# Kernel tuning notes

Hardware: AMD Instinct MI355X
Metric: run time of the kernel (lower is better)

Reference implementation:

```python
import jax, jax.numpy as jnp
import numpy as np

D_MODEL = 1024
N_HEADS = 16
D_HEAD = D_MODEL // N_HEADS
HIDDEN = 4096
B, T = 2, 2048
EPS = 1e-5


def setup_inputs() -> dict:
    key = jax.random.key(0)
    ks = jax.random.split(key, 16)
    s = 0.02
    return {
        "x": jax.random.normal(ks[0], (B, T, D_MODEL), dtype=jnp.float32),
        # LayerNorm 1
        "gamma1": jnp.ones((D_MODEL,), jnp.float32),
        "beta1": jnp.zeros((D_MODEL,), jnp.float32),
        # attention projections, stored (in, out) so y = x @ W + b
        "Wq": jax.random.normal(ks[1], (D_MODEL, D_MODEL), jnp.float32) * s,
        "bq": jnp.zeros((D_MODEL,), jnp.float32),
        "Wk": jax.random.normal(ks[2], (D_MODEL, D_MODEL), jnp.float32) * s,
        "bk": jnp.zeros((D_MODEL,), jnp.float32),
        "Wv": jax.random.normal(ks[3], (D_MODEL, D_MODEL), jnp.float32) * s,
        "bv": jnp.zeros((D_MODEL,), jnp.float32),
        "Wo": jax.random.normal(ks[4], (D_MODEL, D_MODEL), jnp.float32) * s,
        "bo": jnp.zeros((D_MODEL,), jnp.float32),
        # LayerNorm 2
        "gamma2": jnp.ones((D_MODEL,), jnp.float32),
        "beta2": jnp.zeros((D_MODEL,), jnp.float32),
        # MLP
        "W1": jax.random.normal(ks[5], (D_MODEL, HIDDEN), jnp.float32) * s,
        "b1": jnp.zeros((HIDDEN,), jnp.float32),
        "W2": jax.random.normal(ks[6], (HIDDEN, D_MODEL), jnp.float32) * s,
        "b2": jnp.zeros((D_MODEL,), jnp.float32),
    }


def _layernorm(x, gamma, beta):
    mean = jnp.mean(x, axis=-1, keepdims=True)
    var = jnp.mean(jnp.square(x - mean), axis=-1, keepdims=True)  # unbiased=False
    return gamma * (x - mean) * jax.lax.rsqrt(var + EPS) + beta


def _attention(x, Wq, bq, Wk, bk, Wv, bv, Wo, bo):
    b, t, _ = x.shape
    q = (x @ Wq + bq).reshape(b, t, N_HEADS, D_HEAD)
    k = (x @ Wk + bk).reshape(b, t, N_HEADS, D_HEAD)
    v = (x @ Wv + bv).reshape(b, t, N_HEADS, D_HEAD)
    scores = jnp.einsum("bqhd,bkhd->bhqk", q, k) / np.sqrt(D_HEAD).astype(np.float32)
    causal = jnp.tril(jnp.ones((t, t), dtype=bool))  # keep j <= i
    scores = jnp.where(causal, scores, -jnp.inf)
    attn = jax.nn.softmax(scores, axis=-1)
    out = jnp.einsum("bhqk,bkhd->bqhd", attn, v).reshape(b, t, D_MODEL)
    return out @ Wo + bo


def reference(x, gamma1, beta1, Wq, bq, Wk, bk, Wv, bv, Wo, bo,
              gamma2, beta2, W1, b1, W2, b2):
    # x = x + Attn(LN1(x))
    x = x + _attention(_layernorm(x, gamma1, beta1), Wq, bq, Wk, bk, Wv, bv, Wo, bo)
    # x = x + MLP(LN2(x)); torch F.gelu default = exact erf gelu
    h = _layernorm(x, gamma2, beta2)
    h = jax.nn.gelu(h @ W1 + b1, approximate=False) @ W2 + b2
    return x + h
```

## Files before the change

kernel.cpp:

```cpp
#include <hip/hip_runtime.h>
#include <stdint.h>

typedef unsigned short u16;
typedef short bf16x8 __attribute__((ext_vector_type(8)));
typedef float f32x4 __attribute__((ext_vector_type(4)));
typedef float f32x16 __attribute__((ext_vector_type(16)));

#define MB (1024L*1024L)

__device__ inline u16 f2bf(float f) {
  union { float f; unsigned u; } v; v.f = f;
  unsigned r = (v.u + 0x7FFFu + ((v.u >> 16) & 1u)) >> 16;
  return (u16)r;
}

__device__ inline float bf2f(u16 u) {
  union { unsigned u; float f; } v; v.u = ((unsigned)u) << 16; return v.f;
}

__device__ inline unsigned cvtpk(float lo, float hi) {
  unsigned r;
  asm("v_cvt_pk_bf16_f32 %0, %1, %2" : "=v"(r) : "v"(lo), "v"(hi));
  return r;
}

#define GLOAD16(gptr, lptr) \
  __builtin_amdgcn_global_load_lds((__attribute__((address_space(1))) void*)(gptr), \
                                   (__attribute__((address_space(3))) void*)(lptr), 16, 0, 0)

__global__ __launch_bounds__(256) void wprep(
    const float* __restrict__ Wq, const float* __restrict__ Wk,
    const float* __restrict__ Wv, const float* __restrict__ Wo,
    const float* __restrict__ W1, const float* __restrict__ W2,
    const float* __restrict__ bq, const float* __restrict__ bk,
    const float* __restrict__ bv,
    u16* __restrict__ WqkvT, u16* __restrict__ WoT,
    u16* __restrict__ W1T, u16* __restrict__ W2T, float* __restrict__ bqkv,
    const float* __restrict__ x, const float* __restrict__ gamma1,
    const float* __restrict__ beta1, u16* __restrict__ xn) {
  const int blk = blockIdx.x;
  const int tid = threadIdx.x;
  __shared__ float tile[32][33];
  __shared__ float red[8];

  if (blk >= 12292) {
    const int row = blk - 12292;
    const float4 v = *(const float4*)(x + (size_t)row * 1024 + tid * 4);
    float s = v.x + v.y + v.z + v.w;
    float s2 = v.x * v.x + v.y * v.y + v.z * v.z + v.w * v.w;
#pragma unroll
    for (int mm = 1; mm < 64; mm <<= 1) {
      s += __shfl_xor(s, mm, 64);
      s2 += __shfl_xor(s2, mm, 64);
    }
    const int w = tid >> 6;
    if ((tid & 63) == 0) { red[w] = s; red[4 + w] = s2; }
    __syncthreads();
    s = red[0] + red[1] + red[2] + red[3];
    s2 = red[4] + red[5] + red[6] + red[7];
    const float mean = s * (1.0f / 1024.0f);
    const float var = s2 * (1.0f / 1024.0f) - mean * mean;
    const float rstd = rsqrtf(var + 1e-5f);
    const float4 g = *(const float4*)(gamma1 + tid * 4);
    const float4 bb = *(const float4*)(beta1 + tid * 4);
    ushort4 o;
    o.x = f2bf(g.x * (v.x - mean) * rstd + bb.x);
    o.y = f2bf(g.y * (v.y - mean) * rstd + bb.y);
    o.z = f2bf(g.z * (v.z - mean) * rstd + bb.z);
    o.w = f2bf(g.w * (v.w - mean) * rstd + bb.w);
    *(ushort4*)(xn + (size_t)row * 1024 + tid * 4) = o;
    return;
  }
  if (blk >= 12288) {
    int i = (blk - 12288) * 256 + tid;
    bqkv[i] = bq[i]; bqkv[1024 + i] = bk[i]; bqkv[2048 + i] = bv[i];
    return;
  }
  const float* W; u16* WT; int K, N, tb;
  if (blk < 4096) {
    K = 1024; N = 1024;
    if (blk < 1024)      { W = Wq; WT = WqkvT;               tb = blk; }
    else if (blk < 2048) { W = Wk; WT = WqkvT + 1024 * 1024; tb = blk - 1024; }
    else if (blk < 3072) { W = Wv; WT = WqkvT + 2048 * 1024; tb = blk - 2048; }
    else                 { W = Wo; WT = WoT;                 tb = blk - 3072; }
  } else if (blk < 8192) { W = W1; WT = W1T; K = 1024; N = 4096; tb = blk - 4096; }
  else                   { W = W2; WT = W2T; K = 4096; N = 1024; tb = blk - 8192; }

  const int nbn = N >> 5;
  const int bk_ = tb / nbn;
  const int bn = tb % nbn;
  const int r = tid >> 3;
  const int c4 = (tid & 7) << 2;
  const float4 v = *(const float4*)(W + (size_t)(bk_ * 32 + r) * N + bn * 32 + c4);
  tile[r][c4 + 0] = v.x; tile[r][c4 + 1] = v.y;
  tile[r][c4 + 2] = v.z; tile[r][c4 + 3] = v.w;
  __syncthreads();
  ushort4 o;
  o.x = f2bf(tile[c4 + 0][r]); o.y = f2bf(tile[c4 + 1][r]);
  o.z = f2bf(tile[c4 + 2][r]); o.w = f2bf(tile[c4 + 3][r]);
  *(ushort4*)(WT + (size_t)(bn * 32 + r) * K + bk_ * 32 + c4) = o;
}

__global__ __launch_bounds__(256) void ln_kernel(const float* __restrict__ x,
                                                 const float* __restrict__ gamma,
                                                 const float* __restrict__ beta,
                                                 u16* __restrict__ out) {
  const int row = blockIdx.x;
  const int tid = threadIdx.x;
  const float4 v = *(const float4*)(x + (size_t)row * 1024 + tid * 4);
  float s = v.x + v.y + v.z + v.w;
  float s2 = v.x * v.x + v.y * v.y + v.z * v.z + v.w * v.w;
#pragma unroll
  for (int m = 1; m < 64; m <<= 1) {
    s += __shfl_xor(s, m, 64);
    s2 += __shfl_xor(s2, m, 64);
  }
  __shared__ float red[8];
  const int w = tid >> 6;
  if ((tid & 63) == 0) { red[w] = s; red[4 + w] = s2; }
  __syncthreads();
  s = red[0] + red[1] + red[2] + red[3];
  s2 = red[4] + red[5] + red[6] + red[7];
  const float mean = s * (1.0f / 1024.0f);
  const float var = s2 * (1.0f / 1024.0f) - mean * mean;
  const float rstd = rsqrtf(var + 1e-5f);
  const float4 g = *(const float4*)(gamma + tid * 4);
  const float4 b = *(const float4*)(beta + tid * 4);
  ushort4 o;
  o.x = f2bf(g.x * (v.x - mean) * rstd + b.x);
  o.y = f2bf(g.y * (v.y - mean) * rstd + b.y);
  o.z = f2bf(g.z * (v.z - mean) * rstd + b.z);
  o.w = f2bf(g.w * (v.w - mean) * rstd + b.w);
  *(ushort4*)(out + (size_t)row * 1024 + tid * 4) = o;
}

template <int EPI>
__global__ __launch_bounds__(512, 1)
void gemm256sq(const u16* __restrict__ A, const u16* __restrict__ BT,
               const float* __restrict__ bias, void* __restrict__ outp,
               int M, int N, int K) {
  __shared__ __align__(16) u16 As[2][256 * 64];
  __shared__ __align__(16) u16 Bs[2][256 * 64];
  const int nBN = N >> 8;
  const int blk = blockIdx.x;
  const int xcd = blk & 7;
  const int rr = blk >> 3;
  const int bm = xcd * 2 + rr / nBN;
  const int bn = rr % nBN;
  const int tid = threadIdx.x;
  const int lane = tid & 63;
  const int wid = tid >> 6;
  const int wm = wid >> 2;
  const int wn = wid & 3;
  const int e4 = lane >> 4;
  const int l15 = lane & 15;
  const int sx = l15 & 7;

  const int aoffb = (wm * 128 + l15) * 64;
  const int boffb = (wn * 64 + l15) * 64;
  const int ch0 = ((e4 ^ sx) & 7) << 3;
  const int ch1 = (((4 | e4) ^ sx) & 7) << 3;

  size_t gA[2], gB[2]; int lo[2];
#pragma unroll
  for (int c = 0; c < 2; ++c) {
    int idx = tid + (c << 9);
    int rowl = idx >> 3;
    int chg = ((idx & 7) ^ (rowl & 7)) << 3;
    gA[c] = (size_t)(bm * 256 + rowl) * K + chg;
    gB[c] = (size_t)(bn * 256 + rowl) * K + chg;
    lo[c] = idx << 4;
  }
  const size_t hK = (size_t)128 * K;

#define STG_A(tt, h) do { _Pragma("unroll") for (int c = 0; c < 2; ++c) \
  GLOAD16(A + gA[c] + (size_t)(h) * hK + (size_t)(tt) * 64, (char*)As[(tt) & 1] + (h) * 16384 + lo[c]); } while (0)
#define STG_B(tt, h) do { _Pragma("unroll") for (int c = 0; c < 2; ++c) \
  GLOAD16(BT + gB[c] + (size_t)(h) * hK + (size_t)(tt) * 64, (char*)Bs[(tt) & 1] + (h) * 16384 + lo[c]); } while (0)

  f32x4 acc[8][4] = {};
  const int nt = K >> 6;

  STG_A(0, 0); STG_A(0, 1); STG_B(0, 0); STG_B(0, 1);
  STG_B(1, 0); STG_B(1, 1);
  asm volatile("s_waitcnt vmcnt(4)" ::: "memory");
  __builtin_amdgcn_s_barrier();

  for (int t = 0; t < nt; ++t) {
    const u16* Ap = As[t & 1];
    const u16* Bp = Bs[t & 1];
    bf16x8 a[2][4], b01[2][2], b23[2][2];

#pragma unroll
    for (int mm = 0; mm < 4; ++mm) {
      a[0][mm] = *(const bf16x8*)(Ap + aoffb + mm * 1024 + ch0);
      a[1][mm] = *(const bf16x8*)(Ap + aoffb + mm * 1024 + ch1);
    }
#pragma unroll
    for (int nn = 0; nn < 2; ++nn) {
      b01[0][nn] = *(const bf16x8*)(Bp + boffb + nn * 1024 + ch0);
      b01[1][nn] = *(const bf16x8*)(Bp + boffb + nn * 1024 + ch1);
    }
    if (t + 1 < nt) STG_A(t + 1, 0);
    __builtin_amdgcn_s_barrier();
    asm volatile("s_waitcnt lgkmcnt(0)" ::: "memory");
    __builtin_amdgcn_s_setprio(1);
#pragma unroll
    for (int kk = 0; kk < 2; ++kk)
#pragma unroll
      for (int mm = 0; mm < 4; ++mm)
#pragma unroll
        for (int nn = 0; nn < 2; ++nn)
          acc[mm][nn] = __builtin_amdgcn_mfma_f32_16x16x32_bf16(a[kk][mm], b01[kk][nn], acc[mm][nn], 0, 0, 0);
    __builtin_amdgcn_s_setprio(0);
    __builtin_amdgcn_s_barrier();

#pragma unroll
    for (int nn = 0; nn < 2; ++nn) {
      b23[0][nn] = *(const bf16x8*)(Bp + boffb + (2 + nn) * 1024 + ch0);
      b23[1][nn] = *(const bf16x8*)(Bp + boffb + (2 + nn) * 1024 + ch1);
    }
    if (t + 1 < nt) STG_A(t + 1, 1);
    __builtin_amdgcn_s_barrier();
    asm volatile("s_waitcnt lgkmcnt(0)" ::: "memory");
    __builtin_amdgcn_s_setprio(1);
#pragma unroll
    for (int kk = 0; kk < 2; ++kk)
#pragma unroll
      for (int mm = 0; mm < 4; ++mm)
#pragma unroll
        for (int nn = 0; nn < 2; ++nn)
          acc[mm][2 + nn] = __builtin_amdgcn_mfma_f32_16x16x32_bf16(a[kk][mm], b23[kk][nn], acc[mm][2 + nn], 0, 0, 0);
    __builtin_amdgcn_s_setprio(0);
    __builtin_amdgcn_s_barrier();

#pragma unroll
    for (int mm = 0; mm < 4; ++mm) {
      a[0][mm] = *(const bf16x8*)(Ap + aoffb + (4 + mm) * 1024 + ch0);
      a[1][mm] = *(const bf16x8*)(Ap + aoffb + (4 + mm) * 1024 + ch1);
    }
    if (t + 2 < nt) STG_B(t + 2, 0);
    __builtin_amdgcn_s_barrier();
    asm volatile("s_waitcnt lgkmcnt(0)" ::: "memory");
    __builtin_amdgcn_s_setprio(1);
#pragma unroll
    for (int kk = 0; kk < 2; ++kk)
#pragma unroll
      for (int mm = 0; mm < 4; ++mm)
#pragma unroll
        for (int nn = 0; nn < 2; ++nn)
          acc[4 + mm][2 + nn] = __builtin_amdgcn_mfma_f32_16x16x32_bf16(a[kk][mm], b23[kk][nn], acc[4 + mm][2 + nn], 0, 0, 0);
    __builtin_amdgcn_s_setprio(0);
    __builtin_amdgcn_s_barrier();

    if (t + 2 < nt) STG_B(t + 2, 1);
    __builtin_amdgcn_s_barrier();
    __builtin_amdgcn_s_setprio(1);
#pragma unroll
    for (int kk = 0; kk < 2; ++kk)
#pragma unroll
      for (int mm = 0; mm < 4; ++mm)
#pragma unroll
        for (int nn = 0; nn < 2; ++nn)
          acc[4 + mm][nn] = __builtin_amdgcn_mfma_f32_16x16x32_bf16(a[kk][mm], b01[kk][nn], acc[4 + mm][nn], 0, 0, 0);
    __builtin_amdgcn_s_setprio(0);
    if (t + 1 < nt) {
      if (t + 2 < nt) asm volatile("s_waitcnt vmcnt(4)" ::: "memory");
      else            asm volatile("s_waitcnt vmcnt(0)" ::: "memory");
    }
    __builtin_amdgcn_s_barrier();
  }
#undef STG_A
#undef STG_B

  const int rbase = bm * 256 + wm * 128;
  const int cbase = bn * 256 + wn * 64;
#pragma unroll
  for (int m = 0; m < 8; ++m) {
#pragma unroll
    for (int n = 0; n < 4; ++n) {
      const int col = cbase + n * 16 + l15;
      const int row0 = rbase + m * 16 + e4 * 4;
      const float bv = bias[col];
#pragma unroll
      for (int r = 0; r < 4; ++r) {
        const int row = row0 + r;
        float v = acc[m][n][r] + bv;
        if (EPI == 2) {
          float tt = v * (1.0f + 0.044715f * v * v);
          float sg = 1.0f / (1.0f + __expf(-1.5957691216057308f * tt));
          ((u16*)outp)[(size_t)row * N + col] = f2bf(v * sg);
        } else {
          ((u16*)outp)[(size_t)row * N + col] = f2bf(v);
        }
      }
    }
  }
}

template <int EPI, int BN>
__global__ __launch_bounds__(256, (BN == 64) ? 3 : 2)
void gemm_bt(const u16* __restrict__ A, const u16* __restrict__ BT,
             const float* __restrict__ bias, const float* __restrict__ res,
             void* __restrict__ outp, int M, int N, int K) {
  constexpr int MF = (BN == 128) ? 4 : 2;
  constexpr int ACH = 4;
  constexpr int BCH = BN / 32;
  constexpr int LOADS = ACH + BCH;
  __shared__ __align__(16) u16 As[2][128 * 64];
  __shared__ __align__(16) u16 Bs[2][BN * 64];
  const int nBN = N / BN;
  const int hw = blockIdx.x;
  const int xcd = hw & 7;
  const int rr = hw >> 3;
  const int bm = xcd * 4 + rr / nBN;
  const int bn = rr % nBN;
  const int tid = threadIdx.x;
  const int lane = tid & 63;
  const int wid = tid >> 6;
  const int wm = (BN == 128) ? (wid >> 1) : wid;
  const int wn = (BN == 128) ? (wid & 1) : 0;
  const int e4 = lane >> 4;

  int abase[MF], ax[MF];
#pragma unroll
  for (int m = 0; m < MF; ++m) {
    int rowa = wm * (MF * 16) + m * 16 + (lane & 15);
    abase[m] = rowa * 64; ax[m] = rowa & 7;
  }
  int bbase[4], bx[4];
#pragma unroll
  for (int n = 0; n < 4; ++n) {
    int rowb = wn * 64 + n * 16 + (lane & 15);
    bbase[n] = rowb * 64; bx[n] = rowb & 7;
  }

  size_t ga[ACH]; int loa[ACH];
#pragma unroll
  for (int c = 0; c < ACH; ++c) {
    int idx = tid + (c << 8);
    int row = idx >> 3;
    int ch = (idx & 7) ^ (row & 7);
    ga[c] = (size_t)(bm * 128 + row) * K + (ch << 3);
    loa[c] = idx << 4;
  }
  size_t gb[BCH]; int lob[BCH];
#pragma unroll
  for (int c = 0; c < BCH; ++c) {
    int idx = tid + (c << 8);
    int row = idx >> 3;
    int ch = (idx & 7) ^ (row & 7);
    gb[c] = (size_t)(bn * BN + row) * K + (ch << 3);
    lob[c] = idx << 4;
  }

#define STAGE_G(t, bb) do { \
  _Pragma("unroll") for (int c = 0; c < ACH; ++c) \
    GLOAD16(A + ga[c] + (size_t)(t) * 64, (char*)As[bb] + loa[c]); \
  _Pragma("unroll") for (int c = 0; c < BCH; ++c) \
    GLOAD16(BT + gb[c] + (size_t)(t) * 64, (char*)Bs[bb] + lob[c]); \
} while (0)

  f32x4 acc[MF][4] = {};
  const int nt = K >> 6;

  STAGE_G(0, 0);
  STAGE_G(1, 1);

  for (int t = 0; t < nt; ++t) {
    if (t + 1 < nt) {
      asm volatile("s_waitcnt vmcnt(%0)" :: "i"(LOADS) : "memory");
    } else {
      asm volatile("s_waitcnt vmcnt(0)" ::: "memory");
    }
    __builtin_amdgcn_s_barrier();
    const u16* Ap = As[t & 1];
    const u16* Bp = Bs[t & 1];
    bf16x8 af[2][MF], bfr[2][4];
#pragma unroll
    for (int kk = 0; kk < 2; ++kk) {
#pragma unroll
      for (int m = 0; m < MF; ++m)
        af[kk][m] = *(const bf16x8*)(Ap + abase[m] + (((((kk << 2) | e4)) ^ ax[m]) << 3));
#pragma unroll
      for (int n = 0; n < 4; ++n)
        bfr[kk][n] = *(const bf16x8*)(Bp + bbase[n] + (((((kk << 2) | e4)) ^ bx[n]) << 3));
    }
    asm volatile("s_waitcnt lgkmcnt(0)" ::: "memory");
    __builtin_amdgcn_s_barrier();
    if (t + 2 < nt) STAGE_G(t + 2, t & 1);
    __builtin_amdgcn_s_setprio(1);
#pragma unroll
    for (int kk = 0; kk < 2; ++kk)
#pragma unroll
      for (int m = 0; m < MF; ++m)
#pragma unroll
        for (int n = 0; n < 4; ++n)
          acc[m][n] = __builtin_amdgcn_mfma_f32_16x16x32_bf16(af[kk][m], bfr[kk][n], acc[m][n], 0, 0, 0);
    __builtin_amdgcn_s_setprio(0);
  }
#undef STAGE_G

  const int rbase = bm * 128 + wm * (MF * 16);
  const int cbase = bn * BN + wn * 64;
#pragma unroll
  for (int m = 0; m < MF; ++m) {
#pragma unroll
    for (int n = 0; n < 4; ++n) {
      const int col = cbase + n * 16 + (lane & 15);
      const int row0 = rbase + m * 16 + ((lane >> 4) << 2);
      const float bv = bias[col];
#pragma unroll
      for (int r = 0; r < 4; ++r) {
        const int row = row0 + r;
        float v = acc[m][n][r] + bv;
        if (EPI == 1) {
          ((float*)outp)[(size_t)row * N + col] = v + res[(size_t)row * N + col];
        } else if (EPI == 2) {
          float tt = v * (1.0f + 0.044715f * v * v);
          float sg = 1.0f / (1.0f + __expf(-1.5957691216057308f * tt));
          ((u16*)outp)[(size_t)row * N + col] = f2bf(v * sg);
        } else {
          ((u16*)outp)[(size_t)row * N + col] = f2bf(v);
        }
      }
    }
  }
}

__global__ __launch_bounds__(256, 2) void attn_kernel(const u16* __restrict__ QKV,
                                                      u16* __restrict__ O) {
  __shared__ __align__(16) u16 KV[4][4096];
  const int T = 2048, LD = 3072;
  const int blk = blockIdx.x;
  const int xcd = blk & 7;
  const int bh = xcd * 4 + ((blk >> 3) & 3);
  const int c = 15 - (blk >> 5);
  const int b = bh >> 4, hd = bh & 15;
  const int tid = threadIdx.x;
  const int lane = tid & 63;
  const int w = tid >> 6;
  const int h = lane >> 5;
  const int qg = c * 128 + w * 32 + (lane & 31);
  const int diag = 2 * c + (w >> 1);
  const int myNt = diag + 1;
  const int nt = 2 * c + 2;

  const u16* Qb = QKV + (size_t)b * T * LD + hd * 64;
  const u16* Kb = Qb + 1024;
  const u16* Vb = Qb + 2048;

  const float QSC = 0.18033688011112042f;
  bf16x8 qf[4];
#pragma unroll
  for (int s = 0; s < 4; ++s) {
    bf16x8 raw = *(const bf16x8*)(Qb + (size_t)qg * LD + s * 16 + h * 8);
    union { unsigned wd[4]; bf16x8 v; } u;
#pragma unroll
    for (int e = 0; e < 4; ++e)
      u.wd[e] = cvtpk(bf2f((u16)raw[2 * e]) * QSC, bf2f((u16)raw[2 * e + 1]) * QSC);
    qf[s] = u.v;
  }

  union PF { unsigned wd[4]; bf16x8 v; } ONES;
  ONES.wd[0] = 0x3F803F80u; ONES.wd[1] = 0x3F803F80u;
  ONES.wd[2] = 0x3F803F80u; ONES.wd[3] = 0x3F803F80u;

  f32x16 oacc[2] = {};
  f32x16 lacc = {};

  int krow[2], kgc[2], vrow[2], vcol[2];
#pragma unroll
  for (int c2 = 0; c2 < 2; ++c2) {
    int i2 = tid + (c2 << 8);
    krow[c2] = i2 >> 3;
    kgc[c2] = ((i2 & 7) ^ (krow[c2] & 7)) << 3;
    vrow[c2] = i2 >> 3;
    vcol[c2] = i2 & 7;
  }

#define VWRITE(buf, c2, vvreg) do { \
  _Pragma("unroll") for (int e = 0; e < 8; ++e) { \
    int d = vcol[c2] * 8 + e; \
    KV[2 + (buf)][(d << 6) | (vrow[c2] & 7) | ((((vrow[c2] >> 3) ^ e ^ vcol[c2]) & 7) << 3)] = (u16)(vvreg)[e]; \
  } \
} while (0)

#pragma unroll
  for (int c2 = 0; c2 < 2; ++c2) {
    GLOAD16(Kb + (size_t)krow[c2] * LD + kgc[c2], (char*)KV[0] + (tid + (c2 << 8)) * 16);
    bf16x8 vv0 = *(const bf16x8*)(Vb + (size_t)vrow[c2] * LD + vcol[c2] * 8);
    VWRITE(0, c2, vv0);
  }
  __syncthreads();

  int cur = 0;
  for (int j = 0; j < nt; ++j) {
    const bool pre = (j + 1 < nt);
    bf16x8 vv[2];
    if (pre) {
#pragma unroll
      for (int c2 = 0; c2 < 2; ++c2) {
        GLOAD16(Kb + (size_t)((j + 1) * 64 + krow[c2]) * LD + kgc[c2],
                (char*)KV[cur ^ 1] + (tid + (c2 << 8)) * 16);
        vv[c2] = *(const bf16x8*)(Vb + (size_t)((j + 1) * 64 + vrow[c2]) * LD + vcol[c2] * 8);
      }
    }

    if (j < myNt) {
      f32x16 sacc[2];
#pragma unroll
      for (int t = 0; t < 2; ++t)
#pragma unroll
        for (int r = 0; r < 16; ++r) sacc[t][r] = -8.0f;
      const u16* Kp = KV[cur];
      __builtin_amdgcn_s_setprio(1);
#pragma unroll
      for (int t = 0; t < 2; ++t) {
#pragma unroll
        for (int s = 0; s < 4; ++s) {
          int row = t * 32 + (lane & 31);
          bf16x8 kf = *(const bf16x8*)(Kp + (row << 6) + ((((2 * s + h) ^ (row & 7)) & 7) << 3));
          sacc[t] = __builtin_amdgcn_mfma_f32_32x32x16_bf16(kf, qf[s], sacc[t], 0, 0, 0);
        }
      }
      __builtin_amdgcn_s_setprio(0);

      if (j == diag) {
#pragma unroll
        for (int t = 0; t < 2; ++t)
#pragma unroll
          for (int r = 0; r < 16; ++r) {
            int key = (j << 6) + 32 * t + (r & 3) + 8 * (r >> 2) + 4 * h;
            if (key > qg) sacc[t][r] = -200.0f;
          }
      }

#pragma unroll
      for (int t = 0; t < 2; ++t)
#pragma unroll
        for (int r = 0; r < 16; ++r)
          sacc[t][r] = exp2f(sacc[t][r]);

      union PF pf[4];
#pragma unroll
      for (int t = 0; t < 2; ++t) {
#pragma unroll
        for (int kb = 0; kb < 2; ++kb) {
          int base = 8 * kb;
          unsigned A0 = cvtpk(sacc[t][base + 0], sacc[t][base + 1]);
          unsigned A2 = cvtpk(sacc[t][base + 2], sacc[t][base + 3]);
          unsigned A4 = cvtpk(sacc[t][base + 4], sacc[t][base + 5]);
          unsigned A6 = cvtpk(sacc[t][base + 6], sacc[t][base + 7]);
          unsigned S0 = (unsigned)__shfl_xor((int)(h ? A0 : A4), 32, 64);
          unsigned S2 = (unsigned)__shfl_xor((int)(h ? A2 : A6), 32, 64);
          PF& u = pf[2 * t + kb];
          u.wd[0] = h ? S0 : A0;
          u.wd[1] = h ? S2 : A2;
          u.wd[2] = h ? A4 : S0;
          u.wd[3] = h ? A6 : S2;
        }
      }

      const u16* Vp = KV[2 + cur];
      __builtin_amdgcn_s_setprio(1);
#pragma unroll
      for (int ks = 0; ks < 4; ++ks) {
#pragma unroll
        for (int d2 = 0; d2 < 2; ++d2) {
          int d = d2 * 32 + (lane & 31);
          bf16x8 vf = *(const bf16x8*)(Vp + (d << 6) + ((((2 * ks + h) ^ (d & 7) ^ ((d >> 3) & 7)) & 7) << 3));
          oacc[d2] = __builtin_amdgcn_mfma_f32_32x32x16_bf16(vf, pf[ks].v, oacc[d2], 0, 0, 0);
        }
        lacc = __builtin_amdgcn_mfma_f32_32x32x16_bf16(ONES.v, pf[ks].v, lacc, 0, 0, 0);
      }
      __builtin_amdgcn_s_setprio(0);
    }

    if (pre) {
#pragma unroll
      for (int c2 = 0; c2 < 2; ++c2) VWRITE(cur ^ 1, c2, vv[c2]);
    }
    __syncthreads();
    cur ^= 1;
  }
#undef VWRITE

  const float rinv = 1.0f / lacc[0];
  u16* Ob = (u16*)KV;
  const int qloc = w * 32 + (lane & 31);
#pragma unroll
  for (int d2 = 0; d2 < 2; ++d2)
#pragma unroll
    for (int r = 0; r < 16; ++r) {
      int d = d2 * 32 + (r & 3) + 8 * (r >> 2) + 4 * h;
      Ob[(qloc << 6) | (d ^ ((qloc & 7) << 3))] = f2bf(oacc[d2][r] * rinv);
    }
  __syncthreads();
#pragma unroll
  for (int it = 0; it < 4; ++it) {
    int r = (tid >> 3) + it * 32;
    int c8 = tid & 7;
    bf16x8 val = *(const bf16x8*)(Ob + (r << 6) + (((c8 ^ (r & 7)) & 7) << 3));
    int qg2 = c * 128 + r;
    *(bf16x8*)(O + (size_t)(b * T + qg2) * 1024 + hd * 64 + c8 * 8) = val;
  }
}

extern "C" void kernel_launch(void* const* d_in, const int* in_sizes, int n_in,
                              void* d_out, int out_size, void* d_ws, size_t ws_size,
                              hipStream_t stream) {
  const float* x      = (const float*)d_in[0];
  const float* gamma1 = (const float*)d_in[1];
  const float* beta1  = (const float*)d_in[2];
  const float* Wq     = (const float*)d_in[3];
  const float* bq     = (const float*)d_in[4];
  const float* Wk     = (const float*)d_in[5];
  const float* bk     = (const float*)d_in[6];
  const float* Wv     = (const float*)d_in[7];
  const float* bv     = (const float*)d_in[8];
  const float* Wo     = (const float*)d_in[9];
  const float* bo     = (const float*)d_in[10];
  const float* gamma2 = (const float*)d_in[11];
  const float* beta2  = (const float*)d_in[12];
  const float* W1     = (const float*)d_in[13];
  const float* b1     = (const float*)d_in[14];
  const float* W2     = (const float*)d_in[15];
  const float* b2     = (const float*)d_in[16];

  char* ws = (char*)d_ws;
  u16* WqkvT = (u16*)(ws + 0 * MB);
  u16* WoT   = (u16*)(ws + 6 * MB);
  u16* W1T   = (u16*)(ws + 8 * MB);
  u16* W2T   = (u16*)(ws + 16 * MB);
  u16* qkv   = (u16*)(ws + 24 * MB);
  u16* hb    = (u16*)(ws + 24 * MB);
  u16* xn    = (u16*)(ws + 56 * MB);
  float* bqkv = (float*)d_out;
  float* x1 = (float*)d_out;

  const int M = 4096;

  wprep<<<dim3(16388), dim3(256), 0, stream>>>(Wq, Wk, Wv, Wo, W1, W2, bq, bk, bv,
                                               WqkvT, WoT, W1T, W2T, bqkv,
                                               x, gamma1, beta1, xn);

  gemm256sq<0><<<dim3(192), dim3(512), 0, stream>>>(xn, WqkvT, bqkv, qkv, M, 3072, 1024);

  attn_kernel<<<dim3(512), dim3(256), 0, stream>>>(qkv, xn);

  gemm_bt<1, 64><<<dim3(512), dim3(256), 0, stream>>>(xn, WoT, bo, x, x1, M, 1024, 1024);

  ln_kernel<<<dim3(M), dim3(256), 0, stream>>>(x1, gamma2, beta2, xn);

  gemm256sq<2><<<dim3(256), dim3(512), 0, stream>>>(xn, W1T, b1, hb, M, 4096, 1024);
  gemm_bt<1, 64><<<dim3(512), dim3(256), 0, stream>>>(hb, W2T, b2, x1, d_out, M, 1024, 4096);
}
```

Before: 217.5 us.

## Split causal attention KV loop across two blocks and merge partials

Each query chunk's key tiles are split between two blocks by even and odd tile index. This doubles the attention grid for better occupancy and load balance. Because softmax uses a fixed max offset, the unnormalized partial outputs and row sums can be added in a new merge kernel that normalizes and writes the final layout. The score init also seeds the first MFMA with a constant accumulator. The cost is an extra launch, bf16 partial round-trips through memory (reusing d_out as scratch), and some precision loss from storing unnormalized partials in bf16.

```diff
diff --git a/kernel.cpp b/kernel.cpp
--- a/kernel.cpp
+++ b/kernel.cpp
@@ -428,14 +428,18 @@
   }
 }
 
-__global__ __launch_bounds__(256, 2) void attn_kernel(const u16* __restrict__ QKV,
-                                                      u16* __restrict__ O) {
+__global__ __launch_bounds__(256, 2) void attn_split(const u16* __restrict__ QKV,
+                                                     u16* __restrict__ Opart,
+                                                     float* __restrict__ Lpart) {
   __shared__ __align__(16) u16 KV[4][4096];
   const int T = 2048, LD = 3072;
   const int blk = blockIdx.x;
   const int xcd = blk & 7;
-  const int bh = xcd * 4 + ((blk >> 3) & 3);
-  const int c = 15 - (blk >> 5);
+  const int q9 = blk >> 3;
+  const int bh = xcd * 4 + (q9 & 3);
+  const int rest = q9 >> 2;
+  const int s = rest & 1;
+  const int c = 15 - (rest >> 1);
   const int b = bh >> 4, hd = bh & 15;
   const int tid = threadIdx.x;
   const int lane = tid & 63;
@@ -444,7 +448,7 @@
   const int qg = c * 128 + w * 32 + (lane & 31);
   const int diag = 2 * c + (w >> 1);
   const int myNt = diag + 1;
-  const int nt = 2 * c + 2;
+  const int ntc = 2 * c + 2;
 
   const u16* Qb = QKV + (size_t)b * T * LD + hd * 64;
   const u16* Kb = Qb + 1024;
@@ -453,18 +457,22 @@
   const float QSC = 0.18033688011112042f;
   bf16x8 qf[4];
 #pragma unroll
-  for (int s = 0; s < 4; ++s) {
-    bf16x8 raw = *(const bf16x8*)(Qb + (size_t)qg * LD + s * 16 + h * 8);
+  for (int ss = 0; ss < 4; ++ss) {
+    bf16x8 raw = *(const bf16x8*)(Qb + (size_t)qg * LD + ss * 16 + h * 8);
     union { unsigned wd[4]; bf16x8 v; } u;
 #pragma unroll
     for (int e = 0; e < 4; ++e)
       u.wd[e] = cvtpk(bf2f((u16)raw[2 * e]) * QSC, bf2f((u16)raw[2 * e + 1]) * QSC);
-    qf[s] = u.v;
+    qf[ss] = u.v;
   }
 
   union PF { unsigned wd[4]; bf16x8 v; } ONES;
   ONES.wd[0] = 0x3F803F80u; ONES.wd[1] = 0x3F803F80u;
   ONES.wd[2] = 0x3F803F80u; ONES.wd[3] = 0x3F803F80u;
+
+  f32x16 NEG8;
+#pragma unroll
+  for (int r = 0; r < 16; ++r) NEG8[r] = -8.0f;
 
   f32x16 oacc[2] = {};
   f32x16 lacc = {};
@@ -488,40 +496,40 @@
 
 #pragma unroll
   for (int c2 = 0; c2 < 2; ++c2) {
-    GLOAD16(Kb + (size_t)krow[c2] * LD + kgc[c2], (char*)KV[0] + (tid + (c2 << 8)) * 16);
-    bf16x8 vv0 = *(const bf16x8*)(Vb + (size_t)vrow[c2] * LD + vcol[c2] * 8);
+    GLOAD16(Kb + (size_t)(s * 64 + krow[c2]) * LD + kgc[c2], (char*)KV[0] + (tid + (c2 << 8)) * 16);
+    bf16x8 vv0 = *(const bf16x8*)(Vb + (size_t)(s * 64 + vrow[c2]) * LD + vcol[c2] * 8);
     VWRITE(0, c2, vv0);
   }
   __syncthreads();
 
   int cur = 0;
-  for (int j = 0; j < nt; ++j) {
-    const bool pre = (j + 1 < nt);
+  for (int j = s; j < ntc; j += 2) {
+    const bool pre = (j + 2 < ntc);
     bf16x8 vv[2];
     if (pre) {
 #pragma unroll
       for (int c2 = 0; c2 < 2; ++c2) {
-        GLOAD16(Kb + (size_t)((j + 1) * 64 + krow[c2]) * LD + kgc[c2],
+        GLOAD16(Kb + (size_t)((j + 2) * 64 + krow[c2]) * LD + kgc[c2],
                 (char*)KV[cur ^ 1] + (tid + (c2 << 8)) * 16);
-        vv[c2] = *(const bf16x8*)(Vb + (size_t)((j + 1) * 64 + vrow[c2]) * LD + vcol[c2] * 8);
+        vv[c2] = *(const bf16x8*)(Vb + (size_t)((j + 2) * 64 + vrow[c2]) * LD + vcol[c2] * 8);
       }
     }
 
     if (j < myNt) {
       f32x16 sacc[2];
-#pragma unroll
-      for (int t = 0; t < 2; ++t)
-#pragma unroll
-        for (int r = 0; r < 16; ++r) sacc[t][r] = -8.0f;
       const u16* Kp = KV[cur];
       __builtin_amdgcn_s_setprio(1);
 #pragma unroll
       for (int t = 0; t < 2; ++t) {
-#pragma unroll
-        for (int s = 0; s < 4; ++s) {
-          int row = t * 32 + (lane & 31);
-          bf16x8 kf = *(const bf16x8*)(Kp + (row << 6) + ((((2 * s + h) ^ (row & 7)) & 7) << 3));
-          sacc[t] = __builtin_amdgcn_mfma_f32_32x32x16_bf16(kf, qf[s], sacc[t], 0, 0, 0);
+        int row = t * 32 + (lane & 31);
+        {
+          bf16x8 kf = *(const bf16x8*)(Kp + (row << 6) + (((h ^ (row & 7)) & 7) << 3));
+          sacc[t] = __builtin_amdgcn_mfma_f32_32x32x16_bf16(kf, qf[0], NEG8, 0, 0, 0);
+        }
+#pragma unroll
+        for (int ss = 1; ss < 4; ++ss) {
+          bf16x8 kf = *(const bf16x8*)(Kp + (row << 6) + ((((2 * ss + h) ^ (row & 7)) & 7) << 3));
+          sacc[t] = __builtin_amdgcn_mfma_f32_32x32x16_bf16(kf, qf[ss], sacc[t], 0, 0, 0);
         }
       }
       __builtin_amdgcn_s_setprio(0);
@@ -586,25 +594,53 @@
   }
 #undef VWRITE
 
-  const float rinv = 1.0f / lacc[0];
   u16* Ob = (u16*)KV;
   const int qloc = w * 32 + (lane & 31);
+  if (h == 0) Lpart[(size_t)((s * 32 + bh) * 16 + c) * 128 + qloc] = lacc[0];
 #pragma unroll
   for (int d2 = 0; d2 < 2; ++d2)
 #pragma unroll
     for (int r = 0; r < 16; ++r) {
       int d = d2 * 32 + (r & 3) + 8 * (r >> 2) + 4 * h;
-      Ob[(qloc << 6) | (d ^ ((qloc & 7) << 3))] = f2bf(oacc[d2][r] * rinv);
+      Ob[(qloc << 6) | (d ^ ((qloc & 7) << 3))] = f2bf(oacc[d2][r]);
     }
   __syncthreads();
+  const size_t pbase = (size_t)((s * 32 + bh) * 16 + c) * (128 * 64);
 #pragma unroll
   for (int it = 0; it < 4; ++it) {
     int r = (tid >> 3) + it * 32;
     int c8 = tid & 7;
     bf16x8 val = *(const bf16x8*)(Ob + (r << 6) + (((c8 ^ (r & 7)) & 7) << 3));
-    int qg2 = c * 128 + r;
-    *(bf16x8*)(O + (size_t)(b * T + qg2) * 1024 + hd * 64 + c8 * 8) = val;
-  }
+    *(bf16x8*)(Opart + pbase + r * 64 + c8 * 8) = val;
+  }
+}
+
+__global__ __launch_bounds__(256) void attn_merge(const u16* __restrict__ Opart,
+                                                  const float* __restrict__ Lpart,
+                                                  u16* __restrict__ O) {
+  const int rowg = blockIdx.x;
+  const int b = rowg >> 11;
+  const int tt = rowg & 2047;
+  const int c = tt >> 7;
+  const int r = tt & 127;
+  const int t4 = threadIdx.x;
+  const int col = t4 * 4;
+  const int hd = col >> 6;
+  const int d0 = col & 63;
+  const int bh = b * 16 + hd;
+  const size_t i0 = (size_t)((0 * 32 + bh) * 16 + c) * (128 * 64) + r * 64 + d0;
+  const size_t i1 = (size_t)((1 * 32 + bh) * 16 + c) * (128 * 64) + r * 64 + d0;
+  const float l = Lpart[(size_t)((0 * 32 + bh) * 16 + c) * 128 + r] +
+                  Lpart[(size_t)((1 * 32 + bh) * 16 + c) * 128 + r];
+  const float rinv = 1.0f / l;
+  ushort4 a = *(const ushort4*)(Opart + i0);
+  ushort4 bb = *(const ushort4*)(Opart + i1);
+  ushort4 o;
+  o.x = f2bf((bf2f(a.x) + bf2f(bb.x)) * rinv);
+  o.y = f2bf((bf2f(a.y) + bf2f(bb.y)) * rinv);
+  o.z = f2bf((bf2f(a.z) + bf2f(bb.z)) * rinv);
+  o.w = f2bf((bf2f(a.w) + bf2f(bb.w)) * rinv);
+  *(ushort4*)(O + (size_t)rowg * 1024 + col) = o;
 }
 
 extern "C" void kernel_launch(void* const* d_in, const int* in_sizes, int n_in,
@@ -635,8 +671,10 @@
   u16* W2T   = (u16*)(ws + 16 * MB);
   u16* qkv   = (u16*)(ws + 24 * MB);
   u16* hb    = (u16*)(ws + 24 * MB);
+  float* Lpart = (float*)(ws + 48 * MB);
   u16* xn    = (u16*)(ws + 56 * MB);
   float* bqkv = (float*)d_out;
+  u16* Opart = (u16*)d_out;
   float* x1 = (float*)d_out;
 
   const int M = 4096;
@@ -647,7 +685,8 @@
 
   gemm256sq<0><<<dim3(192), dim3(512), 0, stream>>>(xn, WqkvT, bqkv, qkv, M, 3072, 1024);
 
-  attn_kernel<<<dim3(512), dim3(256), 0, stream>>>(qkv, xn);
+  attn_split<<<dim3(1024), dim3(256), 0, stream>>>(qkv, Opart, Lpart);
+  attn_merge<<<dim3(4096), dim3(256), 0, stream>>>(Opart, Lpart, xn);
 
   gemm_bt<1, 64><<<dim3(512), dim3(256), 0, stream>>>(xn, WoT, bo, x, x1, M, 1024, 1024);
 
```

After: 211.5 us (median of 2 runs). -2.8%, faster.
